# Kernel tuning notes

Hardware: AMD Instinct MI355X
Metric: run time of the kernel (lower is better)

Reference implementation:

```python
import jax, jax.numpy as jnp
import numpy as np

D_MODEL = 1024
N_HEADS = 16
HEAD_DIM = D_MODEL // N_HEADS


def setup_inputs() -> dict:
    key = jax.random.key(0)
    ks = jax.random.split(key, 11)
    B, S = 8, 1024
    scale = 1.0 / np.sqrt(D_MODEL)
    inp = {
        "query": jax.random.normal(ks[0], (B, S, D_MODEL), jnp.float32),
        "key": jax.random.normal(ks[1], (B, S, D_MODEL), jnp.float32),
        "value": jax.random.normal(ks[2], (B, S, D_MODEL), jnp.float32),
        "Wq": jax.random.normal(ks[3], (D_MODEL, D_MODEL), jnp.float32) * scale,
        "bq": jnp.zeros((D_MODEL,), jnp.float32),
        "Wk": jax.random.normal(ks[4], (D_MODEL, D_MODEL), jnp.float32) * scale,
        "bk": jnp.zeros((D_MODEL,), jnp.float32),
        "Wv": jax.random.normal(ks[5], (D_MODEL, D_MODEL), jnp.float32) * scale,
        "bv": jnp.zeros((D_MODEL,), jnp.float32),
        "Wo": jax.random.normal(ks[6], (D_MODEL, D_MODEL), jnp.float32) * scale,
        "bo": jnp.zeros((D_MODEL,), jnp.float32),
    }
    return inp


def reference(query, key, value, Wq, bq, Wk, bk, Wv, bv, Wo, bo):
    B, S, _ = query.shape
    # projections (torch Linear: x @ W.T + b)
    Q = query @ Wq.T + bq
    K = key @ Wk.T + bk
    V = value @ Wv.T + bv
    # [B, H, S, Dh]
    Q = Q.reshape(B, S, N_HEADS, HEAD_DIM).transpose(0, 2, 1, 3)
    K = K.reshape(B, S, N_HEADS, HEAD_DIM).transpose(0, 2, 1, 3)
    V = V.reshape(B, S, N_HEADS, HEAD_DIM).transpose(0, 2, 1, 3)
    scores = jnp.einsum("bhqd,bhkd->bhqk", Q, K) / np.sqrt(HEAD_DIM).astype(np.float32)
    attention = jax.nn.softmax(scores, axis=-1)
    context = jnp.einsum("bhqk,bhkd->bhqd", attention, V)
    context = context.transpose(0, 2, 1, 3).reshape(B, S, D_MODEL)
    output = context @ Wo.T + bo
    return output, attention
```

## Files before the change

kernel.cpp:

```cpp
#include <hip/hip_runtime.h>
#include <cstddef>

typedef _Float16 f16;
typedef f16 f16x8 __attribute__((ext_vector_type(8)));
typedef short s16x8 __attribute__((ext_vector_type(8)));
typedef short s16x4 __attribute__((ext_vector_type(4)));
typedef float f32x4 __attribute__((ext_vector_type(4)));

#define S_LEN 1024
#define NH 16
#define HD 64
#define MROWS 8192
#define WPLANE 1048576
#define APLANE 8388608

__device__ __forceinline__ f32x4 mfma_f16(f16x8 a, f16x8 b, f32x4 c) {
  return __builtin_amdgcn_mfma_f32_16x16x32_f16(a, b, c, 0, 0, 0);
}
__device__ __forceinline__ short f2h(float x) {
  f16 h = (f16)x;
  return __builtin_bit_cast(short, h);
}
__device__ __forceinline__ float h2f(short s) {
  return (float)__builtin_bit_cast(f16, s);
}

typedef const __attribute__((address_space(1))) unsigned int* as1_u32p;
typedef __attribute__((address_space(3))) unsigned int* as3_u32p;
__device__ __forceinline__ void gl_lds16(const short* g, short* l) {
  __builtin_amdgcn_global_load_lds((as1_u32p)(const void*)g,
                                   (as3_u32p)(void*)l, 16, 0, 0);
}

__global__ __launch_bounds__(256) void convw4_k(
    const float* __restrict__ W0, const float* __restrict__ W1,
    const float* __restrict__ W2, const float* __restrict__ W3,
    short* __restrict__ out) {
  const int wsel = blockIdx.y;
  const float* W = wsel == 0 ? W0 : (wsel == 1 ? W1 : (wsel == 2 ? W2 : W3));
  const int i = (blockIdx.x * 256 + threadIdx.x) * 8;
  const int n = i >> 10, kg = i & 1023;
  const int dst = (((n >> 7) * 32 + (kg >> 5)) * 128 + (n & 127)) * 32 + (kg & 31);
  float xs[8];
  *(float4*)&xs[0] = *(const float4*)&W[i];
  *(float4*)&xs[4] = *(const float4*)&W[i + 4];
  s16x8 H;
#pragma unroll
  for (int j = 0; j < 8; ++j) H[j] = f2h(xs[j]);
  *(s16x8*)&out[(size_t)wsel * WPLANE + dst] = H;
}

__global__ __launch_bounds__(256) void conva_k(
    const float* __restrict__ A0, const float* __restrict__ A1,
    const float* __restrict__ A2, short* __restrict__ out) {
  const int asel = blockIdx.y;
  const float* A = asel == 0 ? A0 : (asel == 1 ? A1 : A2);
  const int i = (blockIdx.x * 256 + threadIdx.x) * 8;
  const int m = i >> 10, kg = i & 1023;
  const int dst = (((m >> 7) * 32 + (kg >> 5)) * 128 + (m & 127)) * 32 + (kg & 31);
  float xs[8];
  *(float4*)&xs[0] = *(const float4*)&A[i];
  *(float4*)&xs[4] = *(const float4*)&A[i + 4];
  s16x8 H;
#pragma unroll
  for (int j = 0; j < 8; ++j) H[j] = f2h(xs[j]);
  *(s16x8*)&out[(size_t)asel * APLANE + dst] = H;
}

__global__ __launch_bounds__(256, 4) void qkvproj_k(
    const short* __restrict__ Apl, const short* __restrict__ Wpl,
    const float* __restrict__ bq, const float* __restrict__ bk,
    const float* __restrict__ bv, short* __restrict__ Oq,
    short* __restrict__ Ok, short* __restrict__ Ovt) {
  __shared__ __align__(16) short Ah[128][32];
  __shared__ __align__(16) short Bh[128][32];
  const int pid = blockIdx.y;
  const float* bias = pid == 0 ? bq : (pid == 1 ? bk : bv);
  const short* Ahi = Apl + (size_t)pid * APLANE;
  const short* Whi = Wpl + (size_t)pid * WPLANE;

  const int t = threadIdx.x, lane = t & 63, wid = t >> 6;
  const int wr = wid >> 1, wc = wid & 1;
  const int fr = lane & 15, fg = lane >> 4;
  const int bid = blockIdx.x;
  const int wg = (bid & 7) * 64 + (bid >> 3);
  const int bm = (wg >> 3) * 128, bn = (wg & 7) * 128;

  f32x4 acc[4][4] = {};

  for (int ks = 0; ks < 32; ++ks) {
    {
      const size_t boff = ((size_t)(bn >> 7) * 32 + ks) * 4096;
      const size_t aoff = ((size_t)(bm >> 7) * 32 + ks) * 4096;
      const int c0 = wid * 2;
      gl_lds16(&Whi[boff + (size_t)c0 * 512 + lane * 8],       &Bh[0][0] + c0 * 512);
      gl_lds16(&Whi[boff + (size_t)(c0 + 1) * 512 + lane * 8], &Bh[0][0] + (c0 + 1) * 512);
      gl_lds16(&Ahi[aoff + (size_t)c0 * 512 + lane * 8],       &Ah[0][0] + c0 * 512);
      gl_lds16(&Ahi[aoff + (size_t)(c0 + 1) * 512 + lane * 8], &Ah[0][0] + (c0 + 1) * 512);
    }
    __syncthreads();
    f16x8 ah[4], bh[4];
#pragma unroll
    for (int f = 0; f < 4; ++f) {
      ah[f] = *(const f16x8*)&Ah[wr * 64 + f * 16 + fr][fg * 8];
      bh[f] = *(const f16x8*)&Bh[wc * 64 + f * 16 + fr][fg * 8];
    }
#pragma unroll
    for (int i = 0; i < 4; ++i)
#pragma unroll
      for (int j = 0; j < 4; ++j)
        acc[i][j] = mfma_f16(ah[i], bh[j], acc[i][j]);
    __syncthreads();
  }

#pragma unroll
  for (int i = 0; i < 4; ++i) {
#pragma unroll
    for (int j = 0; j < 4; ++j) {
      const int m0 = bm + wr * 64 + i * 16 + fg * 4;
      const int n  = bn + wc * 64 + j * 16 + fr;
      const float bb = bias[n];
      const int batch = m0 >> 10, s0 = m0 & 1023;
      const int h = n >> 6, d = n & 63;
      if (pid < 2) {
        short* O = pid == 0 ? Oq : Ok;
        const size_t base = ((size_t)(batch * NH + h) * S_LEN + s0) * HD + d;
#pragma unroll
        for (int r = 0; r < 4; ++r)
          O[base + (size_t)r * HD] = f2h(acc[i][j][r] + bb);
      } else {
        s16x4 pk;
#pragma unroll
        for (int r = 0; r < 4; ++r) pk[r] = f2h(acc[i][j][r] + bb);
        *(s16x4*)&Ovt[((size_t)(batch * NH + h) * HD + d) * S_LEN + s0] = pk;
      }
    }
  }
}

__global__ __launch_bounds__(256, 2) void oproj_k(
    const short* __restrict__ Ahi, const short* __restrict__ Whi,
    const float* __restrict__ bias, float* __restrict__ Of) {
  __shared__ __align__(16) short Ah[128][32];
  __shared__ __align__(16) short Bh[128][32];
  const int t = threadIdx.x, lane = t & 63, wid = t >> 6;
  const int wr = wid >> 1, wc = wid & 1;
  const int fr = lane & 15, fg = lane >> 4;
  const int bid = blockIdx.x;
  const int wg = (bid & 7) * 64 + (bid >> 3);
  const int bm = (wg >> 3) * 128, bn = (wg & 7) * 128;

  f32x4 acc[4][4] = {};

  for (int ks = 0; ks < 32; ++ks) {
    {
      const size_t boff = ((size_t)(bn >> 7) * 32 + ks) * 4096;
      const size_t aoff = ((size_t)(bm >> 7) * 32 + ks) * 4096;
      const int c0 = wid * 2;
      gl_lds16(&Whi[boff + (size_t)c0 * 512 + lane * 8],       &Bh[0][0] + c0 * 512);
      gl_lds16(&Whi[boff + (size_t)(c0 + 1) * 512 + lane * 8], &Bh[0][0] + (c0 + 1) * 512);
      gl_lds16(&Ahi[aoff + (size_t)c0 * 512 + lane * 8],       &Ah[0][0] + c0 * 512);
      gl_lds16(&Ahi[aoff + (size_t)(c0 + 1) * 512 + lane * 8], &Ah[0][0] + (c0 + 1) * 512);
    }
    __syncthreads();
    f16x8 ah[4], bh[4];
#pragma unroll
    for (int f = 0; f < 4; ++f) {
      ah[f] = *(const f16x8*)&Ah[wr * 64 + f * 16 + fr][fg * 8];
      bh[f] = *(const f16x8*)&Bh[wc * 64 + f * 16 + fr][fg * 8];
    }
#pragma unroll
    for (int i = 0; i < 4; ++i)
#pragma unroll
      for (int j = 0; j < 4; ++j)
        acc[i][j] = mfma_f16(ah[i], bh[j], acc[i][j]);
    __syncthreads();
  }

#pragma unroll
  for (int i = 0; i < 4; ++i) {
#pragma unroll
    for (int j = 0; j < 4; ++j) {
      const int m0 = bm + wr * 64 + i * 16 + fg * 4;
      const int n  = bn + wc * 64 + j * 16 + fr;
      const float bb = bias[n];
#pragma unroll
      for (int r = 0; r < 4; ++r)
        Of[(size_t)(m0 + r) * 1024 + n] = acc[i][j][r] + bb;
    }
  }
}

template <bool FUSE_PV>
__global__ __launch_bounds__(512) void attn_k(
    const short* __restrict__ Qp, const short* __restrict__ Kp,
    const short* __restrict__ Vt, float* __restrict__ attn,
    short* __restrict__ Cp) {
  __shared__ __align__(16) short Kh[64][72];
  __shared__ __align__(16) short Vs[FUSE_PV ? 64 : 1][72];
  __shared__ __align__(16) short Pt[FUSE_PV ? 128 : 1][72];
  __shared__ float sums[2][128];
  __shared__ float sinv[128];

  const int wg = blockIdx.x;
  const int w  = (wg & 7) * 128 + (wg >> 3);
  const int bh = w >> 3;
  const int qb = (w & 7) * 128;
  const int batch = bh >> 4, h = bh & 15;

  const int t = threadIdx.x, lane = t & 63, wid = t >> 6;
  const int wq = wid >> 1, wk = wid & 1;
  const int fr = lane & 15, fg = lane >> 4;
  const int srow = t >> 3, sc = (t & 7) * 8;

  f16x8 qh[2][2];
#pragma unroll
  for (int fm = 0; fm < 2; ++fm)
#pragma unroll
    for (int kc = 0; kc < 2; ++kc) {
      const size_t qa =
          ((size_t)bh * S_LEN + qb + wq * 32 + fm * 16 + fr) * HD + kc * 32 + fg * 8;
      qh[fm][kc] = *(const f16x8*)&Qp[qa];
    }

  float rs[2] = {};
  for (int kt = 0; kt < 16; ++kt) {
    const size_t kb = ((size_t)bh * S_LEN + kt * 64 + srow) * HD + sc;
    *(s16x8*)&Kh[srow][sc] = *(const s16x8*)&Kp[kb];
    __syncthreads();
    f16x8 kh[2][2];
#pragma unroll
    for (int fn = 0; fn < 2; ++fn)
#pragma unroll
      for (int kc = 0; kc < 2; ++kc)
        kh[fn][kc] = *(const f16x8*)&Kh[wk * 32 + fn * 16 + fr][kc * 32 + fg * 8];
    f32x4 s4[2][2] = {};
#pragma unroll
    for (int fn = 0; fn < 2; ++fn)
#pragma unroll
      for (int fm = 0; fm < 2; ++fm)
#pragma unroll
        for (int kc = 0; kc < 2; ++kc)
          s4[fn][fm] = mfma_f16(kh[fn][kc], qh[fm][kc], s4[fn][fm]);
#pragma unroll
    for (int fn = 0; fn < 2; ++fn)
#pragma unroll
      for (int fm = 0; fm < 2; ++fm)
#pragma unroll
        for (int r = 0; r < 4; ++r)
          rs[fm] += __expf(s4[fn][fm][r] * 0.125f);
    __syncthreads();
  }
#pragma unroll
  for (int fm = 0; fm < 2; ++fm) {
    float v = rs[fm];
    v += __shfl_xor(v, 16); v += __shfl_xor(v, 32);
    if (fg == 0) sums[wk][wq * 32 + fm * 16 + fr] = v;
  }
  __syncthreads();
  if (t < 128) sinv[t] = 1.0f / (sums[0][t] + sums[1][t]);
  __syncthreads();

  float pinv[2];
#pragma unroll
  for (int fm = 0; fm < 2; ++fm) pinv[fm] = sinv[wq * 32 + fm * 16 + fr];

  f32x4 apv[2][2] = {};
  for (int kt = 0; kt < 16; ++kt) {
    {
      const size_t kb = ((size_t)bh * S_LEN + kt * 64 + srow) * HD + sc;
      *(s16x8*)&Kh[srow][sc] = *(const s16x8*)&Kp[kb];
      if constexpr (FUSE_PV) {
        const short* vrow = Vt + ((size_t)bh * HD + srow) * S_LEN + kt * 64 + sc;
        *(s16x8*)&Vs[srow][sc] = *(const s16x8*)(vrow);
      }
    }
    __syncthreads();
    f16x8 kh[2][2];
#pragma unroll
    for (int fn = 0; fn < 2; ++fn)
#pragma unroll
      for (int kc = 0; kc < 2; ++kc)
        kh[fn][kc] = *(const f16x8*)&Kh[wk * 32 + fn * 16 + fr][kc * 32 + fg * 8];
    f32x4 s4[2][2] = {};
#pragma unroll
    for (int fn = 0; fn < 2; ++fn)
#pragma unroll
      for (int fm = 0; fm < 2; ++fm)
#pragma unroll
        for (int kc = 0; kc < 2; ++kc)
          s4[fn][fm] = mfma_f16(kh[fn][kc], qh[fm][kc], s4[fn][fm]);
#pragma unroll
    for (int fm = 0; fm < 2; ++fm) {
#pragma unroll
      for (int fn = 0; fn < 2; ++fn) {
        const int kbase = wk * 32 + fn * 16 + fg * 4;
        if constexpr (FUSE_PV) {
          s16x4 pk;
#pragma unroll
          for (int r = 0; r < 4; ++r)
            pk[r] = f2h(__expf(s4[fn][fm][r] * 0.125f) * pinv[fm]);
          *(s16x4*)&Pt[wq * 32 + fm * 16 + fr][kbase] = pk;
        } else {
          const int q = qb + wq * 32 + fm * 16 + fr;
          float4 e4;
          e4.x = __expf(s4[fn][fm][0] * 0.125f) * pinv[fm];
          e4.y = __expf(s4[fn][fm][1] * 0.125f) * pinv[fm];
          e4.z = __expf(s4[fn][fm][2] * 0.125f) * pinv[fm];
          e4.w = __expf(s4[fn][fm][3] * 0.125f) * pinv[fm];
          *(float4*)&attn[((size_t)bh * S_LEN + q) * S_LEN + kt * 64 + kbase] = e4;
        }
      }
    }
    __syncthreads();
    if constexpr (FUSE_PV) {
      {
        const int r0 = t >> 4, c4 = (t & 15) * 4;
#pragma unroll
        for (int it = 0; it < 4; ++it) {
          const int q = r0 + it * 32;
          const s16x4 p4 = *(const s16x4*)&Pt[q][c4];
          float4 o;
          o.x = h2f(p4[0]); o.y = h2f(p4[1]);
          o.z = h2f(p4[2]); o.w = h2f(p4[3]);
          *(float4*)&attn[((size_t)bh * S_LEN + qb + q) * S_LEN + kt * 64 + c4] = o;
        }
      }
      f16x8 af[2][2], bv[2][2];
#pragma unroll
      for (int f = 0; f < 2; ++f)
#pragma unroll
        for (int kc = 0; kc < 2; ++kc) {
          af[f][kc] = *(const f16x8*)&Pt[wq * 32 + f * 16 + fr][kc * 32 + fg * 8];
          bv[f][kc] = *(const f16x8*)&Vs[wk * 32 + f * 16 + fr][kc * 32 + fg * 8];
        }
#pragma unroll
      for (int i = 0; i < 2; ++i)
#pragma unroll
        for (int j = 0; j < 2; ++j)
#pragma unroll
          for (int kc = 0; kc < 2; ++kc)
            apv[i][j] = mfma_f16(af[i][kc], bv[j][kc], apv[i][j]);
      __syncthreads();
    }
  }

  if constexpr (FUSE_PV) {
#pragma unroll
    for (int i = 0; i < 2; ++i)
#pragma unroll
      for (int j = 0; j < 2; ++j) {
        const int s0 = qb + wq * 32 + i * 16 + fg * 4;
        const int d = h * HD + wk * 32 + j * 16 + fr;
#pragma unroll
        for (int r = 0; r < 4; ++r) {
          const int m = batch * S_LEN + s0 + r;
          const size_t idx =
              (((size_t)(m >> 7) * 32 + (d >> 5)) * 128 + (m & 127)) * 32 + (d & 31);
          Cp[idx] = f2h(apv[i][j][r]);
        }
      }
  }
}

__global__ __launch_bounds__(256) void pv2_k(
    const float* __restrict__ attn, const short* __restrict__ Vt,
    short* __restrict__ Cp) {
  __shared__ __align__(16) short At[64][72], Vs[64][72];
  const int wg = blockIdx.x;
  const int w  = (wg & 7) * 256 + (wg >> 3);
  const int bh = w >> 4;
  const int qb = (w & 15) * 64;
  const int batch = bh >> 4, h = bh & 15;
  const int t = threadIdx.x, lane = t & 63, wid = t >> 6;
  const int wq = wid >> 1, wd = wid & 1;
  const int fr = lane & 15, fg = lane >> 4;
  const int srow = t >> 2, sc = (t & 3) * 16;
  const float* arow = attn + ((size_t)bh * S_LEN + qb + srow) * S_LEN + sc;
  const short* vrow = Vt + ((size_t)bh * HD + srow) * S_LEN + sc;

  f32x4 acc[2][2] = {};
  for (int kt = 0; kt < 16; ++kt) {
    float xs[16];
    *(float4*)&xs[0]  = *(const float4*)(arow + kt * 64);
    *(float4*)&xs[4]  = *(const float4*)(arow + kt * 64 + 4);
    *(float4*)&xs[8]  = *(const float4*)(arow + kt * 64 + 8);
    *(float4*)&xs[12] = *(const float4*)(arow + kt * 64 + 12);
    s16x8 c0, c1;
#pragma unroll
    for (int j = 0; j < 8; ++j) { c0[j] = f2h(xs[j]); c1[j] = f2h(xs[8 + j]); }
    const s16x8 v0 = *(const s16x8*)(vrow + kt * 64);
    const s16x8 v1 = *(const s16x8*)(vrow + kt * 64 + 8);
    *(s16x8*)&At[srow][sc] = c0; *(s16x8*)&At[srow][sc + 8] = c1;
    *(s16x8*)&Vs[srow][sc] = v0; *(s16x8*)&Vs[srow][sc + 8] = v1;
    __syncthreads();
    f16x8 af[2][2], bv[2][2];
#pragma unroll
    for (int f = 0; f < 2; ++f)
#pragma unroll
      for (int kc = 0; kc < 2; ++kc) {
        af[f][kc] = *(const f16x8*)&At[wq * 32 + f * 16 + fr][kc * 32 + fg * 8];
        bv[f][kc] = *(const f16x8*)&Vs[wd * 32 + f * 16 + fr][kc * 32 + fg * 8];
      }
#pragma unroll
    for (int i = 0; i < 2; ++i)
#pragma unroll
      for (int j = 0; j < 2; ++j)
#pragma unroll
        for (int kc = 0; kc < 2; ++kc)
          acc[i][j] = mfma_f16(af[i][kc], bv[j][kc], acc[i][j]);
    __syncthreads();
  }

#pragma unroll
  for (int i = 0; i < 2; ++i)
#pragma unroll
    for (int j = 0; j < 2; ++j) {
      const int s0 = qb + wq * 32 + i * 16 + fg * 4;
      const int d = h * HD + wd * 32 + j * 16 + fr;
#pragma unroll
      for (int r = 0; r < 4; ++r) {
        const int m = batch * S_LEN + s0 + r;
        const size_t idx =
            (((size_t)(m >> 7) * 32 + (d >> 5)) * 128 + (m & 127)) * 32 + (d & 31);
        Cp[idx] = f2h(acc[i][j][r]);
      }
    }
}

extern "C" void kernel_launch(void* const* d_in, const int* in_sizes, int n_in,
                              void* d_out, int out_size, void* d_ws, size_t ws_size,
                              hipStream_t stream) {
  const float* query = (const float*)d_in[0];
  const float* key   = (const float*)d_in[1];
  const float* value = (const float*)d_in[2];
  const float* Wq    = (const float*)d_in[3];
  const float* bq    = (const float*)d_in[4];
  const float* Wk    = (const float*)d_in[5];
  const float* bk    = (const float*)d_in[6];
  const float* Wv    = (const float*)d_in[7];
  const float* bv    = (const float*)d_in[8];
  const float* Wo    = (const float*)d_in[9];
  const float* bo    = (const float*)d_in[10];

  float* out  = (float*)d_out;
  float* attn = out + (size_t)MROWS * 1024;

  short* apl = (short*)d_ws;
  short* qp  = apl + 3 * (size_t)APLANE;
  short* kp  = qp + APLANE;
  short* vt  = kp + APLANE;
  short* w4  = vt + APLANE;
  short* cx  = apl + 2 * (size_t)APLANE;

  const dim3 blk(256);

  convw4_k<<<dim3(512, 4), blk, 0, stream>>>(Wq, Wk, Wv, Wo, w4);
  conva_k<<<dim3(4096, 3), blk, 0, stream>>>(query, key, value, apl);
  qkvproj_k<<<dim3(512, 3), blk, 0, stream>>>(apl, w4, bq, bk, bv, qp, kp, vt);

  attn_k<true><<<dim3(1024), dim3(512), 0, stream>>>(qp, kp, vt, attn, cx);

  oproj_k<<<dim3(512), blk, 0, stream>>>(cx, w4 + 3 * WPLANE, bo, out);
}
```

Before: 370.8 us.

## Load K/V fragments directly from global and double-buffer P tile to cut barriers

The attention kernel stops staging K and V tiles through shared memory and loads the MFMA fragments straight from global memory. The P tile becomes double-buffered, which drops the barriers in the sum pass and leaves one barrier per iteration in the PV pass. The unused non-fused template path and the pv2_k kernel are removed. The cost is redundant global/L2 reads: each K and V tile is now fetched by four waves instead of once per block.

```diff
diff --git a/kernel.cpp b/kernel.cpp
--- a/kernel.cpp
+++ b/kernel.cpp
@@ -191,14 +191,11 @@
   }
 }
 
-template <bool FUSE_PV>
 __global__ __launch_bounds__(512) void attn_k(
     const short* __restrict__ Qp, const short* __restrict__ Kp,
     const short* __restrict__ Vt, float* __restrict__ attn,
     short* __restrict__ Cp) {
-  __shared__ __align__(16) short Kh[64][72];
-  __shared__ __align__(16) short Vs[FUSE_PV ? 64 : 1][72];
-  __shared__ __align__(16) short Pt[FUSE_PV ? 128 : 1][72];
+  __shared__ __align__(16) short Pt[2][128][72];
   __shared__ float sums[2][128];
   __shared__ float sinv[128];
 
@@ -211,7 +208,6 @@
   const int t = threadIdx.x, lane = t & 63, wid = t >> 6;
   const int wq = wid >> 1, wk = wid & 1;
   const int fr = lane & 15, fg = lane >> 4;
-  const int srow = t >> 3, sc = (t & 7) * 8;
 
   f16x8 qh[2][2];
 #pragma unroll
@@ -223,17 +219,18 @@
       qh[fm][kc] = *(const f16x8*)&Qp[qa];
     }
 
+  const short* kbp = Kp + ((size_t)bh * S_LEN + wk * 32 + fr) * HD + fg * 8;
+  const short* vbp = Vt + ((size_t)bh * HD + wk * 32 + fr) * S_LEN + fg * 8;
+
   float rs[2] = {};
   for (int kt = 0; kt < 16; ++kt) {
-    const size_t kb = ((size_t)bh * S_LEN + kt * 64 + srow) * HD + sc;
-    *(s16x8*)&Kh[srow][sc] = *(const s16x8*)&Kp[kb];
-    __syncthreads();
+    const short* kp0 = kbp + (size_t)kt * 64 * HD;
     f16x8 kh[2][2];
 #pragma unroll
     for (int fn = 0; fn < 2; ++fn)
 #pragma unroll
       for (int kc = 0; kc < 2; ++kc)
-        kh[fn][kc] = *(const f16x8*)&Kh[wk * 32 + fn * 16 + fr][kc * 32 + fg * 8];
+        kh[fn][kc] = *(const f16x8*)(kp0 + fn * 16 * HD + kc * 32);
     f32x4 s4[2][2] = {};
 #pragma unroll
     for (int fn = 0; fn < 2; ++fn)
@@ -249,7 +246,6 @@
 #pragma unroll
         for (int r = 0; r < 4; ++r)
           rs[fm] += __expf(s4[fn][fm][r] * 0.125f);
-    __syncthreads();
   }
 #pragma unroll
   for (int fm = 0; fm < 2; ++fm) {
@@ -267,21 +263,14 @@
 
   f32x4 apv[2][2] = {};
   for (int kt = 0; kt < 16; ++kt) {
-    {
-      const size_t kb = ((size_t)bh * S_LEN + kt * 64 + srow) * HD + sc;
-      *(s16x8*)&Kh[srow][sc] = *(const s16x8*)&Kp[kb];
-      if constexpr (FUSE_PV) {
-        const short* vrow = Vt + ((size_t)bh * HD + srow) * S_LEN + kt * 64 + sc;
-        *(s16x8*)&Vs[srow][sc] = *(const s16x8*)(vrow);
-      }
-    }
-    __syncthreads();
+    const int b = kt & 1;
+    const short* kp0 = kbp + (size_t)kt * 64 * HD;
     f16x8 kh[2][2];
 #pragma unroll
     for (int fn = 0; fn < 2; ++fn)
 #pragma unroll
       for (int kc = 0; kc < 2; ++kc)
-        kh[fn][kc] = *(const f16x8*)&Kh[wk * 32 + fn * 16 + fr][kc * 32 + fg * 8];
+        kh[fn][kc] = *(const f16x8*)(kp0 + fn * 16 * HD + kc * 32);
     f32x4 s4[2][2] = {};
 #pragma unroll
     for (int fn = 0; fn < 2; ++fn)
@@ -295,121 +284,42 @@
 #pragma unroll
       for (int fn = 0; fn < 2; ++fn) {
         const int kbase = wk * 32 + fn * 16 + fg * 4;
-        if constexpr (FUSE_PV) {
-          s16x4 pk;
-#pragma unroll
-          for (int r = 0; r < 4; ++r)
-            pk[r] = f2h(__expf(s4[fn][fm][r] * 0.125f) * pinv[fm]);
-          *(s16x4*)&Pt[wq * 32 + fm * 16 + fr][kbase] = pk;
-        } else {
-          const int q = qb + wq * 32 + fm * 16 + fr;
-          float4 e4;
-          e4.x = __expf(s4[fn][fm][0] * 0.125f) * pinv[fm];
-          e4.y = __expf(s4[fn][fm][1] * 0.125f) * pinv[fm];
-          e4.z = __expf(s4[fn][fm][2] * 0.125f) * pinv[fm];
-          e4.w = __expf(s4[fn][fm][3] * 0.125f) * pinv[fm];
-          *(float4*)&attn[((size_t)bh * S_LEN + q) * S_LEN + kt * 64 + kbase] = e4;
-        }
-      }
-    }
-    __syncthreads();
-    if constexpr (FUSE_PV) {
-      {
-        const int r0 = t >> 4, c4 = (t & 15) * 4;
-#pragma unroll
-        for (int it = 0; it < 4; ++it) {
-          const int q = r0 + it * 32;
-          const s16x4 p4 = *(const s16x4*)&Pt[q][c4];
-          float4 o;
-          o.x = h2f(p4[0]); o.y = h2f(p4[1]);
-          o.z = h2f(p4[2]); o.w = h2f(p4[3]);
-          *(float4*)&attn[((size_t)bh * S_LEN + qb + q) * S_LEN + kt * 64 + c4] = o;
-        }
-      }
-      f16x8 af[2][2], bv[2][2];
-#pragma unroll
-      for (int f = 0; f < 2; ++f)
-#pragma unroll
-        for (int kc = 0; kc < 2; ++kc) {
-          af[f][kc] = *(const f16x8*)&Pt[wq * 32 + f * 16 + fr][kc * 32 + fg * 8];
-          bv[f][kc] = *(const f16x8*)&Vs[wk * 32 + f * 16 + fr][kc * 32 + fg * 8];
-        }
-#pragma unroll
-      for (int i = 0; i < 2; ++i)
-#pragma unroll
-        for (int j = 0; j < 2; ++j)
-#pragma unroll
-          for (int kc = 0; kc < 2; ++kc)
-            apv[i][j] = mfma_f16(af[i][kc], bv[j][kc], apv[i][j]);
-      __syncthreads();
-    }
-  }
-
-  if constexpr (FUSE_PV) {
+        s16x4 pk;
+#pragma unroll
+        for (int r = 0; r < 4; ++r)
+          pk[r] = f2h(__expf(s4[fn][fm][r] * 0.125f) * pinv[fm]);
+        *(s16x4*)&Pt[b][wq * 32 + fm * 16 + fr][kbase] = pk;
+      }
+    }
+    __syncthreads();
+    {
+      const int r0 = t >> 4, c4 = (t & 15) * 4;
+#pragma unroll
+      for (int it = 0; it < 4; ++it) {
+        const int q = r0 + it * 32;
+        const s16x4 p4 = *(const s16x4*)&Pt[b][q][c4];
+        float4 o;
+        o.x = h2f(p4[0]); o.y = h2f(p4[1]);
+        o.z = h2f(p4[2]); o.w = h2f(p4[3]);
+        *(float4*)&attn[((size_t)bh * S_LEN + qb + q) * S_LEN + kt * 64 + c4] = o;
+      }
+    }
+    f16x8 af[2][2], bv[2][2];
+    const short* vp0 = vbp + kt * 64;
+#pragma unroll
+    for (int f = 0; f < 2; ++f)
+#pragma unroll
+      for (int kc = 0; kc < 2; ++kc) {
+        af[f][kc] = *(const f16x8*)&Pt[b][wq * 32 + f * 16 + fr][kc * 32 + fg * 8];
+        bv[f][kc] = *(const f16x8*)(vp0 + f * 16 * S_LEN + kc * 32);
+      }
 #pragma unroll
     for (int i = 0; i < 2; ++i)
 #pragma unroll
-      for (int j = 0; j < 2; ++j) {
-        const int s0 = qb + wq * 32 + i * 16 + fg * 4;
-        const int d = h * HD + wk * 32 + j * 16 + fr;
-#pragma unroll
-        for (int r = 0; r < 4; ++r) {
-          const int m = batch * S_LEN + s0 + r;
-          const size_t idx =
-              (((size_t)(m >> 7) * 32 + (d >> 5)) * 128 + (m & 127)) * 32 + (d & 31);
-          Cp[idx] = f2h(apv[i][j][r]);
-        }
-      }
-  }
-}
-
-__global__ __launch_bounds__(256) void pv2_k(
-    const float* __restrict__ attn, const short* __restrict__ Vt,
-    short* __restrict__ Cp) {
-  __shared__ __align__(16) short At[64][72], Vs[64][72];
-  const int wg = blockIdx.x;
-  const int w  = (wg & 7) * 256 + (wg >> 3);
-  const int bh = w >> 4;
-  const int qb = (w & 15) * 64;
-  const int batch = bh >> 4, h = bh & 15;
-  const int t = threadIdx.x, lane = t & 63, wid = t >> 6;
-  const int wq = wid >> 1, wd = wid & 1;
-  const int fr = lane & 15, fg = lane >> 4;
-  const int srow = t >> 2, sc = (t & 3) * 16;
-  const float* arow = attn + ((size_t)bh * S_LEN + qb + srow) * S_LEN + sc;
-  const short* vrow = Vt + ((size_t)bh * HD + srow) * S_LEN + sc;
-
-  f32x4 acc[2][2] = {};
-  for (int kt = 0; kt < 16; ++kt) {
-    float xs[16];
-    *(float4*)&xs[0]  = *(const float4*)(arow + kt * 64);
-    *(float4*)&xs[4]  = *(const float4*)(arow + kt * 64 + 4);
-    *(float4*)&xs[8]  = *(const float4*)(arow + kt * 64 + 8);
-    *(float4*)&xs[12] = *(const float4*)(arow + kt * 64 + 12);
-    s16x8 c0, c1;
-#pragma unroll
-    for (int j = 0; j < 8; ++j) { c0[j] = f2h(xs[j]); c1[j] = f2h(xs[8 + j]); }
-    const s16x8 v0 = *(const s16x8*)(vrow + kt * 64);
-    const s16x8 v1 = *(const s16x8*)(vrow + kt * 64 + 8);
-    *(s16x8*)&At[srow][sc] = c0; *(s16x8*)&At[srow][sc + 8] = c1;
-    *(s16x8*)&Vs[srow][sc] = v0; *(s16x8*)&Vs[srow][sc + 8] = v1;
-    __syncthreads();
-    f16x8 af[2][2], bv[2][2];
-#pragma unroll
-    for (int f = 0; f < 2; ++f)
-#pragma unroll
-      for (int kc = 0; kc < 2; ++kc) {
-        af[f][kc] = *(const f16x8*)&At[wq * 32 + f * 16 + fr][kc * 32 + fg * 8];
-        bv[f][kc] = *(const f16x8*)&Vs[wd * 32 + f * 16 + fr][kc * 32 + fg * 8];
-      }
-#pragma unroll
-    for (int i = 0; i < 2; ++i)
-#pragma unroll
       for (int j = 0; j < 2; ++j)
 #pragma unroll
         for (int kc = 0; kc < 2; ++kc)
-          acc[i][j] = mfma_f16(af[i][kc], bv[j][kc], acc[i][j]);
-    __syncthreads();
+          apv[i][j] = mfma_f16(af[i][kc], bv[j][kc], apv[i][j]);
   }
 
 #pragma unroll
@@ -417,13 +327,13 @@
 #pragma unroll
     for (int j = 0; j < 2; ++j) {
       const int s0 = qb + wq * 32 + i * 16 + fg * 4;
-      const int d = h * HD + wd * 32 + j * 16 + fr;
+      const int d = h * HD + wk * 32 + j * 16 + fr;
 #pragma unroll
       for (int r = 0; r < 4; ++r) {
         const int m = batch * S_LEN + s0 + r;
         const size_t idx =
             (((size_t)(m >> 7) * 32 + (d >> 5)) * 128 + (m & 127)) * 32 + (d & 31);
-        Cp[idx] = f2h(acc[i][j][r]);
+        Cp[idx] = f2h(apv[i][j][r]);
       }
     }
 }
@@ -459,7 +369,7 @@
   conva_k<<<dim3(4096, 3), blk, 0, stream>>>(query, key, value, apl);
   qkvproj_k<<<dim3(512, 3), blk, 0, stream>>>(apl, w4, bq, bk, bv, qp, kp, vt);
 
-  attn_k<true><<<dim3(1024), dim3(512), 0, stream>>>(qp, kp, vt, attn, cx);
+  attn_k<<<dim3(1024), dim3(512), 0, stream>>>(qp, kp, vt, attn, cx);
 
   oproj_k<<<dim3(512), blk, 0, stream>>>(cx, w4 + 3 * WPLANE, bo, out);
 }
```

Measured after the change: 430.9 us. 16.2% more time.
